# Kernel tuning notes

Measured on AMD Instinct MI355X. Metric: run time of the kernel, lower is better.

The kernel has to match this reference:

```python
import jax, jax.numpy as jnp
import numpy as np

NUM_CHANNEL_TYPES = 32  # global channel vocabulary (matches fill_max of channel_idx)


def setup_inputs() -> dict:
    key = jax.random.key(0)
    k1, k2, k3, k4, k5, k6 = jax.random.split(key, 6)
    B, C, H, W, E, P = 32, 8, 224, 224, 768, 16
    return {
        "x": jax.random.normal(k1, (B, C, H, W), dtype=jnp.float32),
        "channel_idx": jax.random.randint(k2, (B, C), 0, NUM_CHANNEL_TYPES, dtype=jnp.int64),
        "proj_w": jax.random.normal(k3, (E, P, P), dtype=jnp.float32) * 0.02,
        "proj_b": jax.random.normal(k4, (E,), dtype=jnp.float32) * 0.02,
        "ctx_w": jax.random.normal(k5, (E, E), dtype=jnp.float32) * 0.02,
        "ctx_b": jax.random.normal(k6, (E,), dtype=jnp.float32) * 0.02,
    }


def reference(x, channel_idx, proj_w, proj_b, ctx_w, ctx_b):
    B, C, H, W = x.shape
    E, P, _ = proj_w.shape
    Hp, Wp = H // P, W // P

    # Conv3d(1, E, kernel=(1,P,P), stride=(1,P,P)) == per-channel 2D patchify matmul
    xp = x.reshape(B, C, Hp, P, Wp, P)
    emb = jnp.einsum('bchpwq,epq->bechw', xp, proj_w) + proj_b[None, :, None, None, None]
    # emb: (B, E, C, Hp, Wp)

    # per-(sample, channel) average patch embedding -> (B, C, E)
    av_patch = emb.mean(axis=(3, 4)).transpose(0, 2, 1)
    flat = av_patch.reshape(B * C, E)
    seg = channel_idx.reshape(-1)

    # segment-mean over the batch by channel index (fused scatter-mean)
    sums = jax.ops.segment_sum(flat, seg, num_segments=NUM_CHANNEL_TYPES)
    cnt = jax.ops.segment_sum(jnp.ones((B * C,), flat.dtype), seg, num_segments=NUM_CHANNEL_TYPES)
    means = sums / jnp.maximum(cnt, 1.0)[:, None]
    chan_embed = means[seg].reshape(B, C, E)  # torch computes this under no_grad

    # context projection and broadcast-add back onto patch embeddings
    ctx = chan_embed @ ctx_w.T + ctx_b            # (B, C, E)
    out = emb + ctx.transpose(0, 2, 1)[:, :, :, None, None]

    # flatten(2).transpose(1, 2): (B, C*Hp*Wp, E)
    return out.reshape(B, E, C * Hp * Wp).transpose(0, 2, 1)
```

## Files before the change

kernel.cpp:

```cpp
#include <hip/hip_runtime.h>
#include <hip/hip_bf16.h>

typedef __attribute__((ext_vector_type(8))) short s16x8;
typedef __attribute__((ext_vector_type(4))) float f32x4;
typedef __attribute__((ext_vector_type(8))) unsigned short u16x8;
typedef __attribute__((ext_vector_type(4))) unsigned short u16x4;

static __device__ __forceinline__ unsigned short f2bf(float f) {
  unsigned int u = __float_as_uint(f);
  unsigned int r = u + 0x7fffu + ((u >> 16) & 1u);
  return (unsigned short)(r >> 16);
}
static __device__ __forceinline__ float bf2f(unsigned short s) {
  return __uint_as_float(((unsigned int)s) << 16);
}

static __device__ __forceinline__ void gload16(const void* g, void* l) {
  __builtin_amdgcn_global_load_lds(
      (const __attribute__((address_space(1))) unsigned int*)g,
      (__attribute__((address_space(3))) unsigned int*)l, 16, 0, 0);
}

__global__ __launch_bounds__(256) void k_mega(const float* __restrict__ x,
                                              unsigned short* __restrict__ xbf,
                                              float* __restrict__ avg3,
                                              const float* __restrict__ pw,
                                              unsigned short* __restrict__ pwbf,
                                              const float* __restrict__ cw,
                                              float* __restrict__ cwT) {
  __shared__ __align__(16) char smem[14 * 272 * 2];
  int b = blockIdx.x, t = threadIdx.x;
  if (b < 3584) {
    unsigned short* strip = (unsigned short*)smem;
    int bc = b / 14, hp = b - bc * 14;
    const float* img = x + ((size_t)bc * 224 + hp * 16) * 224;
    for (int idx = t; idx < 896; idx += 256) {
      int row = idx / 56, c4 = idx - row * 56;
      float4 v = reinterpret_cast<const float4*>(img + (size_t)row * 224)[c4];
      int wp = c4 >> 2, q0 = (c4 & 3) << 2;
      u16x4 pk = { f2bf(v.x), f2bf(v.y), f2bf(v.z), f2bf(v.w) };
      *(u16x4*)&strip[wp * 272 + row * 16 + q0] = pk;
    }
    __syncthreads();
    float acc = 0.f;
#pragma unroll
    for (int wp = 0; wp < 14; ++wp) acc += bf2f(strip[wp * 272 + t]);
    avg3[((size_t)bc * 14 + hp) * 256 + t] = acc;
    unsigned short* orow = xbf + ((size_t)bc * 196 + hp * 14) * 256;
    for (int i = t; i < 448; i += 256) {
      int patch = i >> 5, rem = i & 31;
      u16x8 v = *(const u16x8*)&strip[patch * 272 + (rem >> 1) * 16 + (rem & 1) * 8];
      *(u16x8*)(orow + i * 8) = v;
    }
  } else if (b < 3776) {
    int i = (b - 3584) * 256 + t;
    float4 v = reinterpret_cast<const float4*>(pw)[i];
    u16x4 pk = { f2bf(v.x), f2bf(v.y), f2bf(v.z), f2bf(v.w) };
    reinterpret_cast<u16x4*>(pwbf)[i] = pk;
  } else {
    float (*tile)[33] = (float(*)[33])smem;
    int bid2 = b - 3776;
    int bx = bid2 % 24, by = bid2 / 24;
    int tx = t & 31, ty = t >> 5;
#pragma unroll
    for (int k = 0; k < 4; ++k)
      tile[ty + 8 * k][tx] = cw[(size_t)(by * 32 + ty + 8 * k) * 768 + bx * 32 + tx];
    __syncthreads();
#pragma unroll
    for (int k = 0; k < 4; ++k)
      cwT[(size_t)(bx * 32 + ty + 8 * k) * 768 + by * 32 + tx] = tile[tx][ty + 8 * k];
  }
}

__global__ __launch_bounds__(256) void k_segmean(const float* __restrict__ avg3,
                                                 const int* __restrict__ seg,
                                                 float* __restrict__ sp) {
  __shared__ float red[4][64];
  __shared__ int rcnt[4];
  __shared__ int ssg[256];
  int s = blockIdx.x & 31, kc = blockIdx.x >> 5;
  int t = threadIdx.x;
  int kl = t & 63, slice = t >> 6;
  int k = kc * 64 + kl;
  ssg[t] = seg[t];
  __syncthreads();
  float sum = 0.f; int cnt = 0;
  for (int bc = slice * 64; bc < slice * 64 + 64; ++bc) {
    if (ssg[bc] == s) {
      ++cnt;
      const float* row = avg3 + (size_t)bc * 14 * 256 + k;
#pragma unroll
      for (int hp = 0; hp < 14; ++hp) sum += row[hp * 256];
    }
  }
  red[slice][kl] = sum;
  if (kl == 0) rcnt[slice] = cnt;
  __syncthreads();
  if (t < 64) {
    float tot = red[0][t] + red[1][t] + red[2][t] + red[3][t];
    int c = rcnt[0] + rcnt[1] + rcnt[2] + rcnt[3];
    sp[s * 256 + kc * 64 + t] = tot / (196.0f * (float)(c > 0 ? c : 1));
  }
}

__global__ __launch_bounds__(256) void k_means2(const float* __restrict__ sp,
                                                const float* __restrict__ pw,
                                                const float* __restrict__ pb,
                                                float* __restrict__ means) {
  __shared__ float ssp[256];
  __shared__ float red[8][32];
  int s = blockIdx.x & 31, e0 = (blockIdx.x >> 5) << 5;
  int t = threadIdx.x;
  int e = t & 31, ksl = t >> 5;
  ssp[t] = sp[s * 256 + t];
  __syncthreads();
  const float4* w = reinterpret_cast<const float4*>(pw + (size_t)(e0 + e) * 256 + ksl * 32);
  float a = 0.f;
#pragma unroll
  for (int j = 0; j < 8; ++j) {
    float4 v = w[j];
    int kb = ksl * 32 + j * 4;
    a += v.x * ssp[kb] + v.y * ssp[kb + 1] + v.z * ssp[kb + 2] + v.w * ssp[kb + 3];
  }
  red[ksl][e] = a;
  __syncthreads();
  if (t < 32) {
    float tot = 0.f;
#pragma unroll
    for (int j = 0; j < 8; ++j) tot += red[j][t];
    means[s * 768 + e0 + t] = tot + pb[e0 + t];
  }
}

__global__ __launch_bounds__(256) void k_ctx2(const float* __restrict__ means,
                                              const float* __restrict__ cwT,
                                              const float* __restrict__ cb,
                                              const float* __restrict__ pb,
                                              float* __restrict__ addv) {
  __shared__ float mn[768];
  __shared__ float red[8][32];
  int s = blockIdx.x & 31, e0 = (blockIdx.x >> 5) << 5;
  int t = threadIdx.x;
  int e = t & 31, fsl = t >> 5;
  mn[t] = means[s * 768 + t];
  mn[t + 256] = means[s * 768 + 256 + t];
  mn[t + 512] = means[s * 768 + 512 + t];
  __syncthreads();
  const float* col = cwT + (size_t)fsl * 96 * 768 + e0 + e;
  float a = 0.f;
#pragma unroll 8
  for (int j = 0; j < 96; ++j) a += mn[fsl * 96 + j] * col[(size_t)j * 768];
  red[fsl][e] = a;
  __syncthreads();
  if (t < 32) {
    float tot = 0.f;
#pragma unroll
    for (int j = 0; j < 8; ++j) tot += red[j][t];
    addv[s * 768 + e0 + t] = tot + cb[e0 + t] + pb[e0 + t];
  }
}

__global__ __launch_bounds__(512) void k_gemm(
    const unsigned short* __restrict__ xbf, const unsigned short* __restrict__ wbf,
    const float* __restrict__ addv, const int* __restrict__ seg,
    float* __restrict__ out) {
  __shared__ __align__(16) unsigned short Al[128 * 64];
  __shared__ __align__(16) unsigned short Bl[256 * 64];

  int bid = blockIdx.x;
  int xcd = bid & 7, local = bid >> 3;
  int mb = xcd * 49 + local / 3;
  int nb = local - (local / 3) * 3;
  int m0 = mb << 7, n0 = nb << 8;

  int t = threadIdx.x;
  int wave = t >> 6, lane = t & 63;
  int wm = (wave >> 2) << 6, wn = (wave & 3) << 6;
  int lr = lane & 15, hi = lane >> 4;
  int axor = (lr & 7) << 4;

  int swz = (((lane & 7) ^ ((lane >> 3) & 7)) << 4);
  const char* abase = (const char*)xbf + (size_t)(m0 + wave * 16 + (lane >> 3)) * 512 + swz;
  const char* bbase = (const char*)wbf + (size_t)(n0 + wave * 32 + (lane >> 3)) * 512 + swz;
  char* adst = (char*)Al + wave * 2048;
  char* bdst = (char*)Bl + wave * 4096;
  const char* Alc = (const char*)Al;
  const char* Blc = (const char*)Bl;

  f32x4 acc[4][4] = {};

  for (int kt = 0; kt < 4; ++kt) {
    __syncthreads();
#pragma unroll
    for (int i = 0; i < 2; ++i)
      gload16(abase + kt * 128 + i * 4096, adst + i * 1024);
#pragma unroll
    for (int i = 0; i < 4; ++i)
      gload16(bbase + kt * 128 + i * 4096, bdst + i * 1024);
    __syncthreads();
#pragma unroll
    for (int kk = 0; kk < 2; ++kk) {
      s16x8 af[4], bv[4];
      int koff = kk * 64 + hi * 16;
#pragma unroll
      for (int i = 0; i < 4; ++i)
        af[i] = *(const s16x8*)(Alc + (wm + i * 16 + lr) * 128 + (koff ^ axor));
#pragma unroll
      for (int j = 0; j < 4; ++j)
        bv[j] = *(const s16x8*)(Blc + (wn + j * 16 + lr) * 128 + (koff ^ axor));
#pragma unroll
      for (int i = 0; i < 4; ++i)
#pragma unroll
        for (int j = 0; j < 4; ++j)
          acc[i][j] = __builtin_amdgcn_mfma_f32_16x16x32_bf16(bv[j], af[i], acc[i][j], 0, 0, 0);
    }
  }

#pragma unroll
  for (int i = 0; i < 4; ++i) {
    int M = m0 + wm + i * 16 + lr;
    int sgi = seg[M / 196];
    const float* av = addv + (size_t)sgi * 768 + n0 + wn + hi * 4;
    float* orow = out + (size_t)M * 768 + n0 + wn + hi * 4;
#pragma unroll
    for (int j = 0; j < 4; ++j) {
      f32x4 a4 = *(const f32x4*)(av + j * 16);
      f32x4 v = acc[i][j];
      v.x += a4.x; v.y += a4.y; v.z += a4.z; v.w += a4.w;
      *(f32x4*)(orow + j * 16) = v;
    }
  }
}

__global__ void k_cvt_fb(const float* __restrict__ in, unsigned short* __restrict__ o) {
  int i = blockIdx.x * 256 + threadIdx.x;
  float4 v = reinterpret_cast<const float4*>(in)[i];
  u16x4 pk = { f2bf(v.x), f2bf(v.y), f2bf(v.z), f2bf(v.w) };
  reinterpret_cast<u16x4*>(o)[i] = pk;
}

__global__ void k_transpose_fb(const float* __restrict__ in, float* __restrict__ out) {
  __shared__ float tile[32][33];
  int bx = blockIdx.x % 24, by = blockIdx.x / 24;
  int tx = threadIdx.x & 31, ty = threadIdx.x >> 5;
#pragma unroll
  for (int k = 0; k < 4; ++k)
    tile[ty + 8 * k][tx] = in[(size_t)(by * 32 + ty + 8 * k) * 768 + bx * 32 + tx];
  __syncthreads();
#pragma unroll
  for (int k = 0; k < 4; ++k)
    out[(size_t)(bx * 32 + ty + 8 * k) * 768 + by * 32 + tx] = tile[tx][ty + 8 * k];
}

__global__ void k_avgpatch_fb(const float* __restrict__ x, float* __restrict__ avg) {
  int bc = blockIdx.x;
  int k = threadIdx.x;
  int p = k >> 4, q = k & 15;
  const float* base = x + (size_t)bc * 224 * 224;
  float s = 0.f;
  for (int hp = 0; hp < 14; ++hp) {
    const float* row = base + (hp * 16 + p) * 224 + q;
#pragma unroll
    for (int wp = 0; wp < 14; ++wp) s += row[wp * 16];
  }
  avg[bc * 256 + k] = s * (1.0f / 196.0f);
}

__global__ __launch_bounds__(768) void k_chain_fb(const float* __restrict__ avg,
                                                  const int* __restrict__ seg,
                                                  const float* __restrict__ pw,
                                                  const float* __restrict__ pb,
                                                  const float* __restrict__ cwT,
                                                  const float* __restrict__ cb,
                                                  float* __restrict__ addv) {
  __shared__ float sp[256];
  __shared__ float mn[768];
  __shared__ int ssg[256];
  int s = blockIdx.x, t = threadIdx.x;
  if (t < 256) ssg[t] = seg[t];
  __syncthreads();
  if (t < 256) {
    float sum = 0.f; int c = 0;
    for (int bc = 0; bc < 256; ++bc)
      if (ssg[bc] == s) { sum += avg[bc * 256 + t]; ++c; }
    sp[t] = sum / (float)(c > 0 ? c : 1);
  }
  __syncthreads();
  {
    const float4* w = reinterpret_cast<const float4*>(pw + (size_t)t * 256);
    float a = 0.f;
#pragma unroll 8
    for (int k = 0; k < 64; ++k) {
      float4 v = w[k];
      a += v.x * sp[k * 4] + v.y * sp[k * 4 + 1] + v.z * sp[k * 4 + 2] + v.w * sp[k * 4 + 3];
    }
    mn[t] = a + pb[t];
  }
  __syncthreads();
  float a2 = 0.f;
#pragma unroll 8
  for (int f = 0; f < 768; ++f) a2 += mn[f] * cwT[(size_t)f * 768 + t];
  addv[s * 768 + t] = a2 + cb[t] + pb[t];
}

__global__ __launch_bounds__(256) void k_gemm_fb(
    const float* __restrict__ x, const unsigned short* __restrict__ wbf,
    const float* __restrict__ addv, const int* __restrict__ seg,
    float* __restrict__ out) {
  __shared__ unsigned short Al[128][40];
  __shared__ unsigned short Bl[128][40];
  int bid = blockIdx.x;
  int xcd = bid & 7, local = bid >> 3;
  int mb = xcd * 49 + local / 6;
  int nb = local - (local / 6) * 6;
  int m0 = mb << 7, n0 = nb << 7;
  int t = threadIdx.x;
  int wave = t >> 6, lane = t & 63;
  int wm = (wave >> 1) << 6, wn = (wave & 1) << 6;
  int lr = lane & 15, lk = (lane >> 4) << 3;
  int mstage = m0 + (t >> 1);
  int halfA = t & 1;
  int bc = mstage / 196;
  int pij = mstage - bc * 196;
  int hp = pij / 14;
  int wp = pij - hp * 14;
  const float* xbase = x + ((size_t)bc * 224 + hp * 16 + halfA) * 224 + wp * 16;
  const unsigned short* bsrc = wbf + (size_t)(n0 + (t >> 1)) * 256 + halfA * 16;
  unsigned short* adst = &Al[t >> 1][halfA * 16];
  unsigned short* bdst = &Bl[t >> 1][halfA * 16];
  f32x4 acc[4][4] = {};
  for (int ks = 0; ks < 8; ++ks) {
    __syncthreads();
    *(u16x8*)bdst       = *(const u16x8*)(bsrc + ks * 32);
    *(u16x8*)(bdst + 8) = *(const u16x8*)(bsrc + ks * 32 + 8);
    {
      const float4* src = reinterpret_cast<const float4*>(xbase + ks * 448);
      float4 v0 = src[0], v1 = src[1], v2 = src[2], v3 = src[3];
      u16x8 p0 = { f2bf(v0.x), f2bf(v0.y), f2bf(v0.z), f2bf(v0.w),
                   f2bf(v1.x), f2bf(v1.y), f2bf(v1.z), f2bf(v1.w) };
      u16x8 p1 = { f2bf(v2.x), f2bf(v2.y), f2bf(v2.z), f2bf(v2.w),
                   f2bf(v3.x), f2bf(v3.y), f2bf(v3.z), f2bf(v3.w) };
      *(u16x8*)adst = p0;
      *(u16x8*)(adst + 8) = p1;
    }
    __syncthreads();
    s16x8 af[4], bfv[4];
#pragma unroll
    for (int i = 0; i < 4; ++i) af[i] = *(const s16x8*)&Al[wm + i * 16 + lr][lk];
#pragma unroll
    for (int j = 0; j < 4; ++j) bfv[j] = *(const s16x8*)&Bl[wn + j * 16 + lr][lk];
#pragma unroll
    for (int i = 0; i < 4; ++i)
#pragma unroll
      for (int j = 0; j < 4; ++j)
        acc[i][j] = __builtin_amdgcn_mfma_f32_16x16x32_bf16(bfv[j], af[i], acc[i][j], 0, 0, 0);
  }
#pragma unroll
  for (int i = 0; i < 4; ++i) {
    int M = m0 + wm + i * 16 + lr;
    int sgi = seg[M / 196];
    int hi = lane >> 4;
    const float* av = addv + (size_t)sgi * 768 + n0 + wn + hi * 4;
    float* orow = out + (size_t)M * 768 + n0 + wn + hi * 4;
#pragma unroll
    for (int j = 0; j < 4; ++j) {
      f32x4 a4 = *(const f32x4*)(av + j * 16);
      f32x4 v = acc[i][j];
      v.x += a4.x; v.y += a4.y; v.z += a4.z; v.w += a4.w;
      *(f32x4*)(orow + j * 16) = v;
    }
  }
}


extern "C" void kernel_launch(void* const* d_in, const int* in_sizes, int n_in,
                              void* d_out, int out_size, void* d_ws, size_t ws_size,
                              hipStream_t stream) {
  (void)in_sizes; (void)n_in; (void)out_size;
  const float* x  = (const float*)d_in[0];
  const int*   sg = (const int*)d_in[1];
  const float* pw = (const float*)d_in[2];
  const float* pb = (const float*)d_in[3];
  const float* cw = (const float*)d_in[4];
  const float* cb = (const float*)d_in[5];
  float* out = (float*)d_out;

  char* ws = (char*)d_ws;
  unsigned short* pwbf = (unsigned short*)ws;
  float* cwT   = (float*)(ws + 393216);
  float* addv  = (float*)(ws + 2752512);
  float* sp    = (float*)(ws + 2850816);
  float* means = (float*)(ws + 2883584);
  float* avg3  = (float*)(ws + 2981888);
  unsigned short* xbf = (unsigned short*)(ws + 6651904);
  const size_t NEED = 6651904u + 25690112u;

  if (ws_size >= NEED) {
    k_mega<<<4352, 256, 0, stream>>>(x, xbf, avg3, pw, pwbf, cw, cwT);
    k_segmean<<<128, 256, 0, stream>>>(avg3, sg, sp);
    k_means2<<<768, 256, 0, stream>>>(sp, pw, pb, means);
    k_ctx2<<<768, 256, 0, stream>>>(means, cwT, cb, pb, addv);
    k_gemm<<<1176, 512, 0, stream>>>(xbf, pwbf, addv, sg, out);
  } else {
    float* avgp = (float*)(ws + 2981888);
    k_cvt_fb<<<192, 256, 0, stream>>>(pw, pwbf);
    k_transpose_fb<<<576, 256, 0, stream>>>(cw, cwT);
    k_avgpatch_fb<<<256, 256, 0, stream>>>(x, avgp);
    k_chain_fb<<<32, 768, 0, stream>>>(avgp, sg, pw, pb, cwT, cb, addv);
    k_gemm_fb<<<2352, 256, 0, stream>>>(x, pwbf, addv, sg, out);
  }
}
```

Before: 85.20 us.

## Triple-buffer GEMM K-loop with async LDS loads and vmcnt waits

Replaces the single-buffer, two-syncthreads GEMM loop (4 K-tiles of 64) with a three-stage ring of 32-wide K-tiles. Global-to-LDS loads are issued two stages ahead, and the loop waits with explicit vmcnt counts and one barrier per iteration. It also changes the LDS swizzle for the narrower rows and raises wave priority around the MFMA block. The intent is to overlap memory latency with MFMA compute. In exchange the K loop is shorter per iteration, the vmcnt bookkeeping is fragile, and the LDS footprint grows.

```diff
diff --git a/kernel.cpp b/kernel.cpp
--- a/kernel.cpp
+++ b/kernel.cpp
@@ -164,8 +164,8 @@
     const unsigned short* __restrict__ xbf, const unsigned short* __restrict__ wbf,
     const float* __restrict__ addv, const int* __restrict__ seg,
     float* __restrict__ out) {
-  __shared__ __align__(16) unsigned short Al[128 * 64];
-  __shared__ __align__(16) unsigned short Bl[256 * 64];
+  __shared__ __align__(16) unsigned short LA[3][128 * 32];
+  __shared__ __align__(16) unsigned short LB[3][256 * 32];
 
   int bid = blockIdx.x;
   int xcd = bid & 7, local = bid >> 3;
@@ -177,44 +177,54 @@
   int wave = t >> 6, lane = t & 63;
   int wm = (wave >> 2) << 6, wn = (wave & 3) << 6;
   int lr = lane & 15, hi = lane >> 4;
-  int axor = (lr & 7) << 4;
-
-  int swz = (((lane & 7) ^ ((lane >> 3) & 7)) << 4);
-  const char* abase = (const char*)xbf + (size_t)(m0 + wave * 16 + (lane >> 3)) * 512 + swz;
-  const char* bbase = (const char*)wbf + (size_t)(n0 + wave * 32 + (lane >> 3)) * 512 + swz;
-  char* adst = (char*)Al + wave * 2048;
-  char* bdst = (char*)Bl + wave * 4096;
-  const char* Alc = (const char*)Al;
-  const char* Blc = (const char*)Bl;
+
+  int srcq = ((t & 3) ^ ((t >> 3) & 3)) << 4;
+  const char* abase = (const char*)xbf + (size_t)(m0 + (t >> 2)) * 512 + srcq;
+  const char* bbase0 = (const char*)wbf + (size_t)(n0 + (t >> 2)) * 512 + srcq;
+  const char* bbase1 = (const char*)wbf + (size_t)(n0 + 128 + (t >> 2)) * 512 + srcq;
+
+#define STAGE(kt_, buf_)                                             \
+  do {                                                               \
+    gload16(abase + (kt_) * 64, (char*)LA[buf_] + t * 16);           \
+    gload16(bbase0 + (kt_) * 64, (char*)LB[buf_] + t * 16);          \
+    gload16(bbase1 + (kt_) * 64, (char*)LB[buf_] + 8192 + t * 16);   \
+  } while (0)
 
   f32x4 acc[4][4] = {};
 
-  for (int kt = 0; kt < 4; ++kt) {
-    __syncthreads();
-#pragma unroll
-    for (int i = 0; i < 2; ++i)
-      gload16(abase + kt * 128 + i * 4096, adst + i * 1024);
+  STAGE(0, 0);
+  STAGE(1, 1);
+
+  int rq = (hi ^ ((lr >> 1) & 3)) << 4;
+
+#pragma unroll
+  for (int kt = 0; kt < 8; ++kt) {
+    if (kt < 7) {
+      asm volatile("s_waitcnt vmcnt(3)" ::: "memory");
+    } else {
+      asm volatile("s_waitcnt vmcnt(0)" ::: "memory");
+    }
+    __builtin_amdgcn_s_barrier();
+    if (kt + 2 < 8) STAGE(kt + 2, (kt + 2) % 3);
+    int cur = kt % 3;
+    const char* A_ = (const char*)LA[cur];
+    const char* B_ = (const char*)LB[cur];
+    s16x8 af[4], bv[4];
 #pragma unroll
     for (int i = 0; i < 4; ++i)
-      gload16(bbase + kt * 128 + i * 4096, bdst + i * 1024);
-    __syncthreads();
-#pragma unroll
-    for (int kk = 0; kk < 2; ++kk) {
-      s16x8 af[4], bv[4];
-      int koff = kk * 64 + hi * 16;
-#pragma unroll
-      for (int i = 0; i < 4; ++i)
-        af[i] = *(const s16x8*)(Alc + (wm + i * 16 + lr) * 128 + (koff ^ axor));
+      af[i] = *(const s16x8*)(A_ + (wm + i * 16 + lr) * 64 + rq);
+#pragma unroll
+    for (int j = 0; j < 4; ++j)
+      bv[j] = *(const s16x8*)(B_ + (wn + j * 16 + lr) * 64 + rq);
+    __builtin_amdgcn_s_setprio(1);
+#pragma unroll
+    for (int i = 0; i < 4; ++i)
 #pragma unroll
       for (int j = 0; j < 4; ++j)
-        bv[j] = *(const s16x8*)(Blc + (wn + j * 16 + lr) * 128 + (koff ^ axor));
-#pragma unroll
-      for (int i = 0; i < 4; ++i)
-#pragma unroll
-        for (int j = 0; j < 4; ++j)
-          acc[i][j] = __builtin_amdgcn_mfma_f32_16x16x32_bf16(bv[j], af[i], acc[i][j], 0, 0, 0);
-    }
-  }
+        acc[i][j] = __builtin_amdgcn_mfma_f32_16x16x32_bf16(bv[j], af[i], acc[i][j], 0, 0, 0);
+    __builtin_amdgcn_s_setprio(0);
+  }
+#undef STAGE
 
 #pragma unroll
   for (int i = 0; i < 4; ++i) {
```

Measured after the change: 87.26 us. +2.4%, slower.
